# Performance work log

Measured on AMD Instinct MI355X. Metric: run time of the kernel, lower is better.

## Reference

```python
import jax, jax.numpy as jnp
import numpy as np

H = 512  # hidden_size


def setup_inputs() -> dict:
    key = jax.random.key(0)
    ks = jax.random.split(key, 12)
    B, E, S, V = 64, 512, 400, 50000
    s = 1.0 / np.sqrt(H)
    inp = {
        'embedded': jax.random.normal(ks[0], (B, E), jnp.float32),
        'hidden': jax.random.normal(ks[1], (1, B, H), jnp.float32),
        'encoder_states': jax.random.normal(ks[2], (S, B, H), jnp.float32),
        # GRU params (PyTorch layout: gates ordered r,z,n)
        'w_ih': jax.random.uniform(ks[3], (3 * H, E), jnp.float32, -s, s),
        'w_hh': jax.random.uniform(ks[4], (3 * H, H), jnp.float32, -s, s),
        'b_ih': jax.random.uniform(ks[5], (3 * H,), jnp.float32, -s, s),
        'b_hh': jax.random.uniform(ks[6], (3 * H,), jnp.float32, -s, s),
        # nn.Bilinear(H, H, 1)
        'bilin_w': jax.random.uniform(ks[7], (1, H, H), jnp.float32, -s, s),
        'bilin_b': jax.random.uniform(ks[8], (1,), jnp.float32, -s, s),
        # out: Linear(2H, V)
        'out_w': jax.random.uniform(ks[9], (V, 2 * H), jnp.float32, -1.0 / np.sqrt(2 * H), 1.0 / np.sqrt(2 * H)),
        'out_b': jax.random.uniform(ks[10], (V,), jnp.float32, -1.0 / np.sqrt(2 * H), 1.0 / np.sqrt(2 * H)),
    }
    return inp


def reference(embedded, hidden, encoder_states, w_ih, w_hh, b_ih, b_hh,
              bilin_w, bilin_b, out_w, out_b):
    h0 = hidden[0]                                   # [B, H]
    # --- single-step GRU cell (PyTorch gate order r, z, n) ---
    gi = embedded @ w_ih.T + b_ih                    # [B, 3H]
    gh = h0 @ w_hh.T + b_hh                          # [B, 3H]
    r = jax.nn.sigmoid(gi[:, :H] + gh[:, :H])
    z = jax.nn.sigmoid(gi[:, H:2 * H] + gh[:, H:2 * H])
    n = jnp.tanh(gi[:, 2 * H:] + r * gh[:, 2 * H:])
    h_new = (1.0 - z) * n + z * h0                   # [B, H]
    # --- bilinear attention: energy[s,b] = h_new[b] @ W @ enc[s,b] + bias ---
    tmp = h_new @ bilin_w[0]                         # [B, H]
    energy = jnp.einsum('bh,sbh->sb', tmp, encoder_states) + bilin_b[0]  # [S, B]
    attn = jax.nn.softmax(energy, axis=0)            # softmax over source positions
    context = jnp.einsum('sb,sbh->bh', attn, encoder_states)             # [B, H]
    combined = jnp.concatenate([h_new, context], axis=1)                 # [B, 2H]
    logits = combined @ out_w.T + out_b              # [B, V]
    logp = jax.nn.log_softmax(logits, axis=1)
    return logp, h_new[None], attn[:, :, None]
```

## Files before the change

### kernel.cpp

```cpp
#include <hip/hip_runtime.h>
#include <math.h>

static constexpr int H = 512;
static constexpr int B = 64;

typedef __bf16 bf16x8 __attribute__((ext_vector_type(8)));
typedef __bf16 bf16x4 __attribute__((ext_vector_type(4)));
typedef float f32x4 __attribute__((ext_vector_type(4)));

__global__ __launch_bounds__(256) void gemm_mfma_nt(
    const float* __restrict__ A,
    const float* __restrict__ W,
    const float* __restrict__ bias,
    float* __restrict__ C,
    int K, int N, int ldc)
{
    __shared__ __bf16 As[2][64 * 64];
    __shared__ __bf16 Ws[2][64 * 64];

    const int tid  = threadIdx.x;
    const int lane = tid & 63;
    const int wv   = tid >> 6;
    const int n0   = blockIdx.x * 64;

    const int lrow = tid >> 2;
    const int lq   = tid & 3;

    int wrow = n0 + lrow;
    if (wrow > N - 1) wrow = N - 1;
    const float* Aptr = A + (size_t)lrow * K + lq * 16;
    const float* Wptr = W + (size_t)wrow * K + lq * 16;

    f32x4 acc[4] = {};

    float4 ra[4], rw[4];
    #pragma unroll
    for (int i = 0; i < 4; ++i) {
        ra[i] = *(const float4*)(Aptr + 4 * i);
        rw[i] = *(const float4*)(Wptr + 4 * i);
    }

    const int ln = lane & 15;
    const int lk = (lane >> 4) << 3;
    const int NT = K >> 6;

    for (int t = 0; t < NT; ++t) {
        __bf16* a_s = As[t & 1];
        __bf16* w_s = Ws[t & 1];
        #pragma unroll
        for (int i = 0; i < 4; ++i) {
            const int off = ((lrow << 6) + lq * 16 + 4 * i) ^ ((lrow & 7) << 3);
            bf16x4 va = { (__bf16)ra[i].x, (__bf16)ra[i].y, (__bf16)ra[i].z, (__bf16)ra[i].w };
            bf16x4 vw = { (__bf16)rw[i].x, (__bf16)rw[i].y, (__bf16)rw[i].z, (__bf16)rw[i].w };
            *(bf16x4*)&a_s[off] = va;
            *(bf16x4*)&w_s[off] = vw;
        }
        __syncthreads();
        if (t + 1 < NT) {
            const float* Ap = Aptr + (t + 1) * 64;
            const float* Wp = Wptr + (t + 1) * 64;
            #pragma unroll
            for (int i = 0; i < 4; ++i) {
                ra[i] = *(const float4*)(Ap + 4 * i);
                rw[i] = *(const float4*)(Wp + 4 * i);
            }
        }
        bf16x8 bfrag[2];
        #pragma unroll
        for (int ks = 0; ks < 2; ++ks) {
            const int row = wv * 16 + ln;
            const int off = ((row << 6) + ks * 32 + lk) ^ ((row & 7) << 3);
            bfrag[ks] = *(bf16x8*)&w_s[off];
        }
        #pragma unroll
        for (int m = 0; m < 4; ++m) {
            const int row = m * 16 + ln;
            #pragma unroll
            for (int ks = 0; ks < 2; ++ks) {
                const int off = ((row << 6) + ks * 32 + lk) ^ ((row & 7) << 3);
                bf16x8 afrag = *(bf16x8*)&a_s[off];
                acc[m] = __builtin_amdgcn_mfma_f32_16x16x32_bf16(afrag, bfrag[ks], acc[m], 0, 0, 0);
            }
        }
    }

    const int col = n0 + wv * 16 + ln;
    if (col < N) {
        const float bv = bias ? bias[col] : 0.f;
        #pragma unroll
        for (int m = 0; m < 4; ++m) {
            const int rbase = m * 16 + (lane >> 4) * 4;
            #pragma unroll
            for (int j = 0; j < 4; ++j)
                C[(size_t)(rbase + j) * ldc + col] = acc[m][j] + bv;
        }
    }
}

__global__ __launch_bounds__(256) void gemm_a64_kn(
    const float* __restrict__ A, const float* __restrict__ W,
    float* __restrict__ C, int K, int N, int ldc)
{
    __shared__ float As[64][68];
    __shared__ float Bs[64][68];
    const int tid = threadIdx.x;
    const int n0 = blockIdx.x * 64;
    const int tv = tid & 15;
    const int tb = tid >> 4;
    const int lrow = tid >> 2;
    const int lk0  = (tid & 3) * 16;

    float acc[4][4] = {{0.f, 0.f, 0.f, 0.f}};

    for (int kc = 0; kc < K; kc += 64) {
        #pragma unroll
        for (int i = 0; i < 4; ++i) {
            const float4 a = *(const float4*)(A + (size_t)lrow * K + kc + lk0 + 4 * i);
            As[lk0 + 4 * i + 0][lrow] = a.x;
            As[lk0 + 4 * i + 1][lrow] = a.y;
            As[lk0 + 4 * i + 2][lrow] = a.z;
            As[lk0 + 4 * i + 3][lrow] = a.w;
        }
        {
            const int v  = tid & 63;
            const int kg = tid >> 6;
            #pragma unroll
            for (int i = 0; i < 16; ++i) {
                const int kk = kg * 16 + i;
                Bs[kk][v] = (n0 + v < N) ? W[(size_t)(kc + kk) * N + n0 + v] : 0.f;
            }
        }
        __syncthreads();
        #pragma unroll 16
        for (int kk = 0; kk < 64; ++kk) {
            const float4 a = *(const float4*)&As[kk][tb * 4];
            const float4 b = *(const float4*)&Bs[kk][tv * 4];
            acc[0][0] += a.x * b.x; acc[0][1] += a.x * b.y; acc[0][2] += a.x * b.z; acc[0][3] += a.x * b.w;
            acc[1][0] += a.y * b.x; acc[1][1] += a.y * b.y; acc[1][2] += a.y * b.z; acc[1][3] += a.y * b.w;
            acc[2][0] += a.z * b.x; acc[2][1] += a.z * b.y; acc[2][2] += a.z * b.z; acc[2][3] += a.z * b.w;
            acc[3][0] += a.w * b.x; acc[3][1] += a.w * b.y; acc[3][2] += a.w * b.z; acc[3][3] += a.w * b.w;
        }
        __syncthreads();
    }
    #pragma unroll
    for (int i = 0; i < 4; ++i) {
        const int bb = tb * 4 + i;
        #pragma unroll
        for (int j = 0; j < 4; ++j) {
            const int n = n0 + tv * 4 + j;
            if (n < N) C[(size_t)bb * ldc + n] = acc[i][j];
        }
    }
}

__global__ __launch_bounds__(512) void gru_gates(
    const float* __restrict__ gi, const float* __restrict__ gh,
    const float* __restrict__ h0, float* __restrict__ hnew,
    float* __restrict__ combined)
{
    const int b = blockIdx.x;
    const int h = threadIdx.x;
    const size_t o = (size_t)b * 3 * H;
    const float r = 1.f / (1.f + expf(-(gi[o + h] + gh[o + h])));
    const float z = 1.f / (1.f + expf(-(gi[o + H + h] + gh[o + H + h])));
    const float n = tanhf(gi[o + 2 * H + h] + r * gh[o + 2 * H + h]);
    const float hn = (1.f - z) * n + z * h0[(size_t)b * H + h];
    hnew[(size_t)b * H + h] = hn;
    combined[(size_t)b * 2 * H + h] = hn;
}

__global__ __launch_bounds__(256) void energy_k(
    const float* __restrict__ tmp, const float* __restrict__ enc,
    const float* __restrict__ bilin_b, float* __restrict__ energy, int S)
{
    const int gw = (int)((blockIdx.x * 256 + threadIdx.x) >> 6);
    const int lane = threadIdx.x & 63;
    if (gw >= S * B) return;
    const int s = gw >> 6;
    const int b = gw & 63;
    const float* e = enc + ((size_t)s * B + b) * H;
    const float* t = tmp + (size_t)b * H;
    const int k0 = lane * 8;
    const float4 e0 = *(const float4*)(e + k0);
    const float4 e1 = *(const float4*)(e + k0 + 4);
    const float4 t0 = *(const float4*)(t + k0);
    const float4 t1 = *(const float4*)(t + k0 + 4);
    float p = e0.x * t0.x + e0.y * t0.y + e0.z * t0.z + e0.w * t0.w
            + e1.x * t1.x + e1.y * t1.y + e1.z * t1.z + e1.w * t1.w;
    #pragma unroll
    for (int off = 32; off; off >>= 1) p += __shfl_down(p, off);
    if (lane == 0) energy[(size_t)s * B + b] = p + bilin_b[0];
}

__global__ __launch_bounds__(128) void softmax_s(
    const float* __restrict__ energy, float* __restrict__ attn, int S)
{
    const int b = blockIdx.x;
    const int t = threadIdx.x;
    __shared__ float w0[2], w1[2];
    float m = -1e30f;
    for (int s = t; s < S; s += 128) m = fmaxf(m, energy[(size_t)s * B + b]);
    #pragma unroll
    for (int off = 32; off; off >>= 1) m = fmaxf(m, __shfl_xor(m, off));
    if ((t & 63) == 0) w0[t >> 6] = m;
    __syncthreads();
    m = fmaxf(w0[0], w0[1]);
    float sum = 0.f;
    for (int s = t; s < S; s += 128) sum += expf(energy[(size_t)s * B + b] - m);
    #pragma unroll
    for (int off = 32; off; off >>= 1) sum += __shfl_xor(sum, off);
    if ((t & 63) == 0) w1[t >> 6] = sum;
    __syncthreads();
    const float inv = 1.f / (w1[0] + w1[1]);
    for (int s = t; s < S; s += 128)
        attn[(size_t)s * B + b] = expf(energy[(size_t)s * B + b] - m) * inv;
}

static constexpr int CSP = 8;
__global__ __launch_bounds__(512) void context_part(
    const float* __restrict__ attn, const float* __restrict__ enc,
    float* __restrict__ part, int S, int chunk)
{
    const int b = blockIdx.x;
    const int p = blockIdx.y;
    const int h = threadIdx.x;
    const int s0 = p * chunk;
    int s1 = s0 + chunk; if (s1 > S) s1 = S;
    __shared__ float a_s[128];
    if (h < s1 - s0) a_s[h] = attn[(size_t)(s0 + h) * B + b];
    __syncthreads();
    float c = 0.f;
    const float* e = enc + ((size_t)s0 * B + b) * H + h;
    for (int s = s0; s < s1; ++s, e += (size_t)B * H)
        c += a_s[s - s0] * (*e);
    part[((size_t)p * B + b) * H + h] = c;
}

__global__ __launch_bounds__(512) void context_reduce(
    const float* __restrict__ part, float* __restrict__ combined)
{
    const int b = blockIdx.x;
    const int h = threadIdx.x;
    float c = 0.f;
    #pragma unroll
    for (int p = 0; p < CSP; ++p) c += part[((size_t)p * B + b) * H + h];
    combined[(size_t)b * 2 * H + H + h] = c;
}

static constexpr int LSP = 16;
__global__ __launch_bounds__(256) void lsm_part(
    const float* __restrict__ logits, float* __restrict__ pm,
    float* __restrict__ ps, int V)
{
    const int b = blockIdx.x;
    const int p = blockIdx.y;
    const int t = threadIdx.x;
    const int V4 = V >> 2;
    const int chunk = (V4 + LSP - 1) / LSP;
    const int i0 = p * chunk;
    int i1 = i0 + chunk; if (i1 > V4) i1 = V4;
    const float4* row = (const float4*)(logits + (size_t)b * V);
    __shared__ float sm[4], ss[4];

    float m = -1e30f;
    for (int i = i0 + t; i < i1; i += 256) {
        const float4 v = row[i];
        m = fmaxf(fmaxf(fmaxf(m, v.x), v.y), fmaxf(v.z, v.w));
    }
    #pragma unroll
    for (int off = 32; off; off >>= 1) m = fmaxf(m, __shfl_xor(m, off));
    if ((t & 63) == 0) sm[t >> 6] = m;
    __syncthreads();
    m = fmaxf(fmaxf(sm[0], sm[1]), fmaxf(sm[2], sm[3]));

    float s = 0.f;
    for (int i = i0 + t; i < i1; i += 256) {
        const float4 v = row[i];
        s += expf(v.x - m) + expf(v.y - m) + expf(v.z - m) + expf(v.w - m);
    }
    #pragma unroll
    for (int off = 32; off; off >>= 1) s += __shfl_xor(s, off);
    if ((t & 63) == 0) ss[t >> 6] = s;
    __syncthreads();
    if (t == 0) {
        pm[b * LSP + p] = m;
        ps[b * LSP + p] = ss[0] + ss[1] + ss[2] + ss[3];
    }
}

__global__ __launch_bounds__(64) void lsm_combine(
    const float* __restrict__ pm, const float* __restrict__ ps,
    float* __restrict__ c)
{
    const int b = blockIdx.x;
    const int l = threadIdx.x;
    float m = (l < LSP) ? pm[b * LSP + l] : -1e30f;
    float mm = m;
    #pragma unroll
    for (int off = 32; off; off >>= 1) mm = fmaxf(mm, __shfl_xor(mm, off));
    float s = (l < LSP) ? ps[b * LSP + l] * expf(m - mm) : 0.f;
    #pragma unroll
    for (int off = 32; off; off >>= 1) s += __shfl_xor(s, off);
    if (l == 0) c[b] = mm + logf(s);
}

__global__ __launch_bounds__(256) void lsm_apply(
    float* __restrict__ logits, const float* __restrict__ c, int V)
{
    const int b = blockIdx.y;
    const int i = blockIdx.x * 256 + threadIdx.x;
    const int V4 = V >> 2;
    if (i >= V4) return;
    float4* row = (float4*)(logits + (size_t)b * V);
    float4 v = row[i];
    const float cb = c[b];
    v.x -= cb; v.y -= cb; v.z -= cb; v.w -= cb;
    row[i] = v;
}

extern "C" void kernel_launch(void* const* d_in, const int* in_sizes, int n_in,
                              void* d_out, int out_size, void* d_ws, size_t ws_size,
                              hipStream_t stream)
{
    const float* embedded = (const float*)d_in[0];
    const float* hidden   = (const float*)d_in[1];
    const float* enc      = (const float*)d_in[2];
    const float* w_ih     = (const float*)d_in[3];
    const float* w_hh     = (const float*)d_in[4];
    const float* b_ih     = (const float*)d_in[5];
    const float* b_hh     = (const float*)d_in[6];
    const float* bilin_w  = (const float*)d_in[7];
    const float* bilin_b  = (const float*)d_in[8];
    const float* out_w    = (const float*)d_in[9];
    const float* out_b    = (const float*)d_in[10];
    float* out = (float*)d_out;

    const int E = in_sizes[0] / B;
    const int S = in_sizes[2] / (B * H);
    const int V = in_sizes[9] / (2 * H);

    float* logp = out;
    float* hnew = out + (size_t)B * V;
    float* attn = hnew + (size_t)B * H;

    float* ws       = (float*)d_ws;
    float* gi       = ws;
    float* gh       = gi + (size_t)B * 3 * H;
    float* tmp      = gh + (size_t)B * 3 * H;
    float* energy   = tmp + (size_t)B * H;
    float* combined = energy + (size_t)S * B;
    float* part     = combined + (size_t)B * 2 * H;
    float* pm       = part + (size_t)CSP * B * H;
    float* ps       = pm + (size_t)B * LSP;
    float* cb       = ps + (size_t)B * LSP;

    gemm_mfma_nt<<<(3 * H) / 64, 256, 0, stream>>>(embedded, w_ih, b_ih, gi, E, 3 * H, 3 * H);
    gemm_mfma_nt<<<(3 * H) / 64, 256, 0, stream>>>(hidden, w_hh, b_hh, gh, H, 3 * H, 3 * H);

    gru_gates<<<B, H, 0, stream>>>(gi, gh, hidden, hnew, combined);

    gemm_a64_kn<<<H / 64, 256, 0, stream>>>(hnew, bilin_w, tmp, H, H, H);

    energy_k<<<(S * B + 3) / 4, 256, 0, stream>>>(tmp, enc, bilin_b, energy, S);

    softmax_s<<<B, 128, 0, stream>>>(energy, attn, S);

    const int chunk = (S + CSP - 1) / CSP;
    context_part<<<dim3(B, CSP), 512, 0, stream>>>(attn, enc, part, S, chunk);
    context_reduce<<<B, 512, 0, stream>>>(part, combined);

    gemm_mfma_nt<<<(V + 63) / 64, 256, 0, stream>>>(combined, out_w, out_b, logp, 2 * H, V, V);

    lsm_part<<<dim3(B, LSP), 256, 0, stream>>>(logp, pm, ps, V);
    lsm_combine<<<B, 64, 0, stream>>>(pm, ps, cb);
    lsm_apply<<<dim3((V / 4 + 255) / 256, B), 256, 0, stream>>>(logp, cb, V);
}
```

Baseline: 178.9 us.

## Fuse GRU gemms with gates, flash-style attention, wider output GEMM tile

The two GRU gate GEMMs and the gate elementwise kernel become one kernel that accumulates r, z and n tiles directly. Energy, softmax and context become a single online-softmax pass over encoder states, split into partitions, followed by a combine kernel, so the encoder tensor is read once instead of twice. The vocabulary projection GEMM now uses 128-column tiles to reuse the A tile across more outputs, and the log-softmax split count is raised. The GRU kernel loses double buffering and runs on only 8 blocks, and the flash kernel uses 64-thread blocks, which may underuse the GPU.

New measurement: 202.2 us. 1.13x slower.

```diff
diff --git a/kernel.cpp b/kernel.cpp
--- a/kernel.cpp
+++ b/kernel.cpp
@@ -3,96 +3,100 @@
 
 static constexpr int H = 512;
 static constexpr int B = 64;
+static constexpr int P = 32;
+static constexpr int LSP = 32;
 
 typedef __bf16 bf16x8 __attribute__((ext_vector_type(8)));
 typedef __bf16 bf16x4 __attribute__((ext_vector_type(4)));
 typedef float f32x4 __attribute__((ext_vector_type(4)));
 
-__global__ __launch_bounds__(256) void gemm_mfma_nt(
-    const float* __restrict__ A,
-    const float* __restrict__ W,
-    const float* __restrict__ bias,
-    float* __restrict__ C,
-    int K, int N, int ldc)
-{
-    __shared__ __bf16 As[2][64 * 64];
-    __shared__ __bf16 Ws[2][64 * 64];
-
-    const int tid  = threadIdx.x;
+__device__ __forceinline__ float sigmoidf_(float x) { return 1.f / (1.f + expf(-x)); }
+
+__global__ __launch_bounds__(256) void gru_fused(
+    const float* __restrict__ X, const float* __restrict__ Hp,
+    const float* __restrict__ w_ih, const float* __restrict__ w_hh,
+    const float* __restrict__ b_ih, const float* __restrict__ b_hh,
+    float* __restrict__ hnew, float* __restrict__ combined)
+{
+    __shared__ __bf16 As[64 * 64];
+    __shared__ __bf16 Wr[64 * 64];
+    __shared__ __bf16 Wz[64 * 64];
+    __shared__ __bf16 Wn[64 * 64];
+    const int tid = threadIdx.x;
     const int lane = tid & 63;
-    const int wv   = tid >> 6;
-    const int n0   = blockIdx.x * 64;
-
+    const int wv = tid >> 6;
+    const int c0 = blockIdx.x * 64;
     const int lrow = tid >> 2;
-    const int lq   = tid & 3;
-
-    int wrow = n0 + lrow;
-    if (wrow > N - 1) wrow = N - 1;
-    const float* Aptr = A + (size_t)lrow * K + lq * 16;
-    const float* Wptr = W + (size_t)wrow * K + lq * 16;
-
-    f32x4 acc[4] = {};
-
-    float4 ra[4], rw[4];
-    #pragma unroll
-    for (int i = 0; i < 4; ++i) {
-        ra[i] = *(const float4*)(Aptr + 4 * i);
-        rw[i] = *(const float4*)(Wptr + 4 * i);
-    }
-
+    const int lq = tid & 3;
     const int ln = lane & 15;
     const int lk = (lane >> 4) << 3;
-    const int NT = K >> 6;
-
-    for (int t = 0; t < NT; ++t) {
-        __bf16* a_s = As[t & 1];
-        __bf16* w_s = Ws[t & 1];
-        #pragma unroll
-        for (int i = 0; i < 4; ++i) {
-            const int off = ((lrow << 6) + lq * 16 + 4 * i) ^ ((lrow & 7) << 3);
-            bf16x4 va = { (__bf16)ra[i].x, (__bf16)ra[i].y, (__bf16)ra[i].z, (__bf16)ra[i].w };
-            bf16x4 vw = { (__bf16)rw[i].x, (__bf16)rw[i].y, (__bf16)rw[i].z, (__bf16)rw[i].w };
-            *(bf16x4*)&a_s[off] = va;
-            *(bf16x4*)&w_s[off] = vw;
-        }
-        __syncthreads();
-        if (t + 1 < NT) {
-            const float* Ap = Aptr + (t + 1) * 64;
-            const float* Wp = Wptr + (t + 1) * 64;
+
+    f32x4 acc_r[4] = {}, acc_z[4] = {}, acc_n[2][4] = {};
+
+    #pragma unroll
+    for (int ph = 0; ph < 2; ++ph) {
+        const float* a_src = ph ? Hp : X;
+        const float* w_src = ph ? w_hh : w_ih;
+        const float* Ap = a_src + (size_t)lrow * H + lq * 16;
+        const float* Rp = w_src + (size_t)(c0 + lrow) * H + lq * 16;
+        const float* Zp = w_src + (size_t)(H + c0 + lrow) * H + lq * 16;
+        const float* Np = w_src + (size_t)(2 * H + c0 + lrow) * H + lq * 16;
+        for (int t = 0; t < H / 64; ++t) {
+            __syncthreads();
             #pragma unroll
             for (int i = 0; i < 4; ++i) {
-                ra[i] = *(const float4*)(Ap + 4 * i);
-                rw[i] = *(const float4*)(Wp + 4 * i);
-            }
-        }
-        bf16x8 bfrag[2];
-        #pragma unroll
-        for (int ks = 0; ks < 2; ++ks) {
-            const int row = wv * 16 + ln;
-            const int off = ((row << 6) + ks * 32 + lk) ^ ((row & 7) << 3);
-            bfrag[ks] = *(bf16x8*)&w_s[off];
-        }
-        #pragma unroll
-        for (int m = 0; m < 4; ++m) {
-            const int row = m * 16 + ln;
+                const int off = ((lrow << 6) + lq * 16 + 4 * i) ^ ((lrow & 7) << 3);
+                const float4 va = *(const float4*)(Ap + t * 64 + 4 * i);
+                const float4 vr = *(const float4*)(Rp + t * 64 + 4 * i);
+                const float4 vz = *(const float4*)(Zp + t * 64 + 4 * i);
+                const float4 vn = *(const float4*)(Np + t * 64 + 4 * i);
+                *(bf16x4*)&As[off] = bf16x4{ (__bf16)va.x, (__bf16)va.y, (__bf16)va.z, (__bf16)va.w };
+                *(bf16x4*)&Wr[off] = bf16x4{ (__bf16)vr.x, (__bf16)vr.y, (__bf16)vr.z, (__bf16)vr.w };
+                *(bf16x4*)&Wz[off] = bf16x4{ (__bf16)vz.x, (__bf16)vz.y, (__bf16)vz.z, (__bf16)vz.w };
+                *(bf16x4*)&Wn[off] = bf16x4{ (__bf16)vn.x, (__bf16)vn.y, (__bf16)vn.z, (__bf16)vn.w };
+            }
+            __syncthreads();
+            bf16x8 br[2], bz[2], bn[2];
             #pragma unroll
             for (int ks = 0; ks < 2; ++ks) {
+                const int row = wv * 16 + ln;
                 const int off = ((row << 6) + ks * 32 + lk) ^ ((row & 7) << 3);
-                bf16x8 afrag = *(bf16x8*)&a_s[off];
-                acc[m] = __builtin_amdgcn_mfma_f32_16x16x32_bf16(afrag, bfrag[ks], acc[m], 0, 0, 0);
-            }
-        }
-    }
-
-    const int col = n0 + wv * 16 + ln;
-    if (col < N) {
-        const float bv = bias ? bias[col] : 0.f;
-        #pragma unroll
-        for (int m = 0; m < 4; ++m) {
-            const int rbase = m * 16 + (lane >> 4) * 4;
-            #pragma unroll
-            for (int j = 0; j < 4; ++j)
-                C[(size_t)(rbase + j) * ldc + col] = acc[m][j] + bv;
+                br[ks] = *(bf16x8*)&Wr[off];
+                bz[ks] = *(bf16x8*)&Wz[off];
+                bn[ks] = *(bf16x8*)&Wn[off];
+            }
+            #pragma unroll
+            for (int m = 0; m < 4; ++m) {
+                const int row = m * 16 + ln;
+                #pragma unroll
+                for (int ks = 0; ks < 2; ++ks) {
+                    const int off = ((row << 6) + ks * 32 + lk) ^ ((row & 7) << 3);
+                    const bf16x8 af = *(bf16x8*)&As[off];
+                    acc_r[m]     = __builtin_amdgcn_mfma_f32_16x16x32_bf16(af, br[ks], acc_r[m], 0, 0, 0);
+                    acc_z[m]     = __builtin_amdgcn_mfma_f32_16x16x32_bf16(af, bz[ks], acc_z[m], 0, 0, 0);
+                    acc_n[ph][m] = __builtin_amdgcn_mfma_f32_16x16x32_bf16(af, bn[ks], acc_n[ph][m], 0, 0, 0);
+                }
+            }
+        }
+    }
+
+    const int h = c0 + wv * 16 + ln;
+    const float br_ = b_ih[h] + b_hh[h];
+    const float bz_ = b_ih[H + h] + b_hh[H + h];
+    const float bni = b_ih[2 * H + h];
+    const float bnh = b_hh[2 * H + h];
+    #pragma unroll
+    for (int m = 0; m < 4; ++m) {
+        #pragma unroll
+        for (int j = 0; j < 4; ++j) {
+            const int b = m * 16 + (lane >> 4) * 4 + j;
+            const float r = sigmoidf_(acc_r[m][j] + br_);
+            const float z = sigmoidf_(acc_z[m][j] + bz_);
+            const float n = tanhf(acc_n[0][m][j] + bni + r * (acc_n[1][m][j] + bnh));
+            const float h0v = Hp[(size_t)b * H + h];
+            const float hn = (1.f - z) * n + z * h0v;
+            hnew[(size_t)b * H + h] = hn;
+            combined[(size_t)b * 2 * H + h] = hn;
         }
     }
 }
@@ -153,101 +157,175 @@
     }
 }
 
-__global__ __launch_bounds__(512) void gru_gates(
-    const float* __restrict__ gi, const float* __restrict__ gh,
-    const float* __restrict__ h0, float* __restrict__ hnew,
-    float* __restrict__ combined)
+__global__ __launch_bounds__(64) void flash_part(
+    const float* __restrict__ tmp, const float* __restrict__ enc,
+    const float* __restrict__ bilin_b, float* __restrict__ energy,
+    float* __restrict__ ctxp, float* __restrict__ mp, float* __restrict__ lp,
+    int S)
 {
     const int b = blockIdx.x;
-    const int h = threadIdx.x;
-    const size_t o = (size_t)b * 3 * H;
-    const float r = 1.f / (1.f + expf(-(gi[o + h] + gh[o + h])));
-    const float z = 1.f / (1.f + expf(-(gi[o + H + h] + gh[o + H + h])));
-    const float n = tanhf(gi[o + 2 * H + h] + r * gh[o + 2 * H + h]);
-    const float hn = (1.f - z) * n + z * h0[(size_t)b * H + h];
-    hnew[(size_t)b * H + h] = hn;
-    combined[(size_t)b * 2 * H + h] = hn;
-}
-
-__global__ __launch_bounds__(256) void energy_k(
-    const float* __restrict__ tmp, const float* __restrict__ enc,
-    const float* __restrict__ bilin_b, float* __restrict__ energy, int S)
-{
-    const int gw = (int)((blockIdx.x * 256 + threadIdx.x) >> 6);
-    const int lane = threadIdx.x & 63;
-    if (gw >= S * B) return;
-    const int s = gw >> 6;
-    const int b = gw & 63;
-    const float* e = enc + ((size_t)s * B + b) * H;
-    const float* t = tmp + (size_t)b * H;
-    const int k0 = lane * 8;
-    const float4 e0 = *(const float4*)(e + k0);
-    const float4 e1 = *(const float4*)(e + k0 + 4);
-    const float4 t0 = *(const float4*)(t + k0);
-    const float4 t1 = *(const float4*)(t + k0 + 4);
-    float p = e0.x * t0.x + e0.y * t0.y + e0.z * t0.z + e0.w * t0.w
-            + e1.x * t1.x + e1.y * t1.y + e1.z * t1.z + e1.w * t1.w;
-    #pragma unroll
-    for (int off = 32; off; off >>= 1) p += __shfl_down(p, off);
-    if (lane == 0) energy[(size_t)s * B + b] = p + bilin_b[0];
-}
-
-__global__ __launch_bounds__(128) void softmax_s(
-    const float* __restrict__ energy, float* __restrict__ attn, int S)
+    const int p = blockIdx.y;
+    const int ln = threadIdx.x;
+    const int k0 = ln * 8;
+
+    const float4 t0 = *(const float4*)(tmp + (size_t)b * H + k0);
+    const float4 t1 = *(const float4*)(tmp + (size_t)b * H + k0 + 4);
+    const float bb = bilin_b[0];
+
+    float m = -1e30f, l = 0.f;
+    float4 c0 = {0.f, 0.f, 0.f, 0.f}, c1 = {0.f, 0.f, 0.f, 0.f};
+
+    for (int s = p; s < S; s += P) {
+        const float* e = enc + ((size_t)s * B + b) * H + k0;
+        const float4 e0 = *(const float4*)(e);
+        const float4 e1 = *(const float4*)(e + 4);
+        float d = e0.x * t0.x + e0.y * t0.y + e0.z * t0.z + e0.w * t0.w
+                + e1.x * t1.x + e1.y * t1.y + e1.z * t1.z + e1.w * t1.w;
+        #pragma unroll
+        for (int off = 32; off; off >>= 1) d += __shfl_xor(d, off);
+        const float E = d + bb;
+        if (ln == 0) energy[(size_t)s * B + b] = E;
+        const float mn = fmaxf(m, E);
+        const float sc = expf(m - mn);
+        const float w  = expf(E - mn);
+        l = l * sc + w;
+        c0.x = c0.x * sc + w * e0.x; c0.y = c0.y * sc + w * e0.y;
+        c0.z = c0.z * sc + w * e0.z; c0.w = c0.w * sc + w * e0.w;
+        c1.x = c1.x * sc + w * e1.x; c1.y = c1.y * sc + w * e1.y;
+        c1.z = c1.z * sc + w * e1.z; c1.w = c1.w * sc + w * e1.w;
+        m = mn;
+    }
+    float* cp = ctxp + ((size_t)b * P + p) * H + k0;
+    *(float4*)cp = c0;
+    *(float4*)(cp + 4) = c1;
+    if (ln == 0) { mp[b * P + p] = m; lp[b * P + p] = l; }
+}
+
+__global__ __launch_bounds__(256) void attn_combine(
+    const float* __restrict__ mp, const float* __restrict__ lp,
+    const float* __restrict__ ctxp, const float* __restrict__ energy,
+    float* __restrict__ combined, float* __restrict__ attn, int S)
 {
     const int b = blockIdx.x;
     const int t = threadIdx.x;
-    __shared__ float w0[2], w1[2];
-    float m = -1e30f;
-    for (int s = t; s < S; s += 128) m = fmaxf(m, energy[(size_t)s * B + b]);
-    #pragma unroll
-    for (int off = 32; off; off >>= 1) m = fmaxf(m, __shfl_xor(m, off));
-    if ((t & 63) == 0) w0[t >> 6] = m;
+    __shared__ float sm_[P], sl_[P], sc_[P];
+    if (t < P) { sm_[t] = mp[b * P + t]; sl_[t] = lp[b * P + t]; }
     __syncthreads();
-    m = fmaxf(w0[0], w0[1]);
-    float sum = 0.f;
-    for (int s = t; s < S; s += 128) sum += expf(energy[(size_t)s * B + b] - m);
-    #pragma unroll
-    for (int off = 32; off; off >>= 1) sum += __shfl_xor(sum, off);
-    if ((t & 63) == 0) w1[t >> 6] = sum;
+    float M = -1e30f;
+    #pragma unroll
+    for (int p = 0; p < P; ++p) M = fmaxf(M, sm_[p]);
+    if (t < P) sc_[t] = expf(sm_[t] - M);
     __syncthreads();
-    const float inv = 1.f / (w1[0] + w1[1]);
-    for (int s = t; s < S; s += 128)
-        attn[(size_t)s * B + b] = expf(energy[(size_t)s * B + b] - m) * inv;
-}
-
-static constexpr int CSP = 8;
-__global__ __launch_bounds__(512) void context_part(
-    const float* __restrict__ attn, const float* __restrict__ enc,
-    float* __restrict__ part, int S, int chunk)
-{
-    const int b = blockIdx.x;
-    const int p = blockIdx.y;
-    const int h = threadIdx.x;
-    const int s0 = p * chunk;
-    int s1 = s0 + chunk; if (s1 > S) s1 = S;
-    __shared__ float a_s[128];
-    if (h < s1 - s0) a_s[h] = attn[(size_t)(s0 + h) * B + b];
-    __syncthreads();
-    float c = 0.f;
-    const float* e = enc + ((size_t)s0 * B + b) * H + h;
-    for (int s = s0; s < s1; ++s, e += (size_t)B * H)
-        c += a_s[s - s0] * (*e);
-    part[((size_t)p * B + b) * H + h] = c;
-}
-
-__global__ __launch_bounds__(512) void context_reduce(
-    const float* __restrict__ part, float* __restrict__ combined)
-{
-    const int b = blockIdx.x;
-    const int h = threadIdx.x;
-    float c = 0.f;
-    #pragma unroll
-    for (int p = 0; p < CSP; ++p) c += part[((size_t)p * B + b) * H + h];
-    combined[(size_t)b * 2 * H + H + h] = c;
-}
-
-static constexpr int LSP = 16;
+    float L = 0.f;
+    #pragma unroll
+    for (int p = 0; p < P; ++p) L += sl_[p] * sc_[p];
+    const float invL = 1.f / L;
+
+    for (int h = t; h < H; h += 256) {
+        float acc = 0.f;
+        #pragma unroll
+        for (int p = 0; p < P; ++p)
+            acc += ctxp[((size_t)b * P + p) * H + h] * sc_[p];
+        combined[(size_t)b * 2 * H + H + h] = acc * invL;
+    }
+    for (int s = t; s < S; s += 256)
+        attn[(size_t)s * B + b] = expf(energy[(size_t)s * B + b] - M) * invL;
+}
+
+__global__ __launch_bounds__(256) void gemm_mfma_nt128(
+    const float* __restrict__ A,
+    const float* __restrict__ W,
+    const float* __restrict__ bias,
+    float* __restrict__ C, int K, int N, int ldc)
+{
+    __shared__ __bf16 As[2][64 * 64];
+    __shared__ __bf16 Ws[2][128 * 64];
+
+    const int tid = threadIdx.x;
+    const int lane = tid & 63;
+    const int wv = tid >> 6;
+    const int n0 = blockIdx.x * 128;
+
+    const int arow = tid >> 2, aq = tid & 3;
+    const int wrow = tid >> 1, wh = tid & 1;
+    int wr = n0 + wrow;
+    if (wr > N - 1) wr = N - 1;
+    const float* Aptr = A + (size_t)arow * K + aq * 16;
+    const float* Wptr = W + (size_t)wr * K + wh * 32;
+
+    f32x4 acc[4][2] = {};
+    float4 ra[4], rw[8];
+    #pragma unroll
+    for (int i = 0; i < 4; ++i) ra[i] = *(const float4*)(Aptr + 4 * i);
+    #pragma unroll
+    for (int i = 0; i < 8; ++i) rw[i] = *(const float4*)(Wptr + 4 * i);
+
+    const int ln = lane & 15;
+    const int lk = (lane >> 4) << 3;
+    const int NT = K >> 6;
+
+    for (int t = 0; t < NT; ++t) {
+        __bf16* a_s = As[t & 1];
+        __bf16* w_s = Ws[t & 1];
+        #pragma unroll
+        for (int i = 0; i < 4; ++i) {
+            const int off = ((arow << 6) + aq * 16 + 4 * i) ^ ((arow & 7) << 3);
+            *(bf16x4*)&a_s[off] = bf16x4{ (__bf16)ra[i].x, (__bf16)ra[i].y, (__bf16)ra[i].z, (__bf16)ra[i].w };
+        }
+        #pragma unroll
+        for (int i = 0; i < 8; ++i) {
+            const int off = ((wrow << 6) + wh * 32 + 4 * i) ^ ((wrow & 7) << 3);
+            *(bf16x4*)&w_s[off] = bf16x4{ (__bf16)rw[i].x, (__bf16)rw[i].y, (__bf16)rw[i].z, (__bf16)rw[i].w };
+        }
+        __syncthreads();
+        if (t + 1 < NT) {
+            const float* Ap = Aptr + (t + 1) * 64;
+            const float* Wp = Wptr + (t + 1) * 64;
+            #pragma unroll
+            for (int i = 0; i < 4; ++i) ra[i] = *(const float4*)(Ap + 4 * i);
+            #pragma unroll
+            for (int i = 0; i < 8; ++i) rw[i] = *(const float4*)(Wp + 4 * i);
+        }
+        bf16x8 bfrag[2][2];
+        #pragma unroll
+        for (int nf = 0; nf < 2; ++nf) {
+            #pragma unroll
+            for (int ks = 0; ks < 2; ++ks) {
+                const int row = wv * 32 + nf * 16 + ln;
+                const int off = ((row << 6) + ks * 32 + lk) ^ ((row & 7) << 3);
+                bfrag[nf][ks] = *(bf16x8*)&w_s[off];
+            }
+        }
+        #pragma unroll
+        for (int m = 0; m < 4; ++m) {
+            const int row = m * 16 + ln;
+            #pragma unroll
+            for (int ks = 0; ks < 2; ++ks) {
+                const int off = ((row << 6) + ks * 32 + lk) ^ ((row & 7) << 3);
+                const bf16x8 af = *(bf16x8*)&a_s[off];
+                #pragma unroll
+                for (int nf = 0; nf < 2; ++nf)
+                    acc[m][nf] = __builtin_amdgcn_mfma_f32_16x16x32_bf16(af, bfrag[nf][ks], acc[m][nf], 0, 0, 0);
+            }
+        }
+    }
+
+    #pragma unroll
+    for (int nf = 0; nf < 2; ++nf) {
+        const int col = n0 + wv * 32 + nf * 16 + ln;
+        if (col < N) {
+            const float bv = bias[col];
+            #pragma unroll
+            for (int m = 0; m < 4; ++m) {
+                const int rbase = m * 16 + (lane >> 4) * 4;
+                #pragma unroll
+                for (int j = 0; j < 4; ++j)
+                    C[(size_t)(rbase + j) * ldc + col] = acc[m][nf][j] + bv;
+            }
+        }
+    }
+}
+
 __global__ __launch_bounds__(256) void lsm_part(
     const float* __restrict__ logits, float* __restrict__ pm,
     float* __restrict__ ps, int V)
@@ -335,7 +413,6 @@
     const float* out_b    = (const float*)d_in[10];
     float* out = (float*)d_out;
 
-    const int E = in_sizes[0] / B;
     const int S = in_sizes[2] / (B * H);
     const int V = in_sizes[9] / (2 * H);
 
@@ -344,32 +421,25 @@
     float* attn = hnew + (size_t)B * H;
 
     float* ws       = (float*)d_ws;
-    float* gi       = ws;
-    float* gh       = gi + (size_t)B * 3 * H;
-    float* tmp      = gh + (size_t)B * 3 * H;
+    float* tmp      = ws;
     float* energy   = tmp + (size_t)B * H;
     float* combined = energy + (size_t)S * B;
-    float* part     = combined + (size_t)B * 2 * H;
-    float* pm       = part + (size_t)CSP * B * H;
+    float* ctxp     = combined + (size_t)B * 2 * H;
+    float* mp       = ctxp + (size_t)B * P * H;
+    float* lp       = mp + (size_t)B * P;
+    float* pm       = lp + (size_t)B * P;
     float* ps       = pm + (size_t)B * LSP;
     float* cb       = ps + (size_t)B * LSP;
 
-    gemm_mfma_nt<<<(3 * H) / 64, 256, 0, stream>>>(embedded, w_ih, b_ih, gi, E, 3 * H, 3 * H);
-    gemm_mfma_nt<<<(3 * H) / 64, 256, 0, stream>>>(hidden, w_hh, b_hh, gh, H, 3 * H, 3 * H);
-
-    gru_gates<<<B, H, 0, stream>>>(gi, gh, hidden, hnew, combined);
+    gru_fused<<<H / 64, 256, 0, stream>>>(embedded, hidden, w_ih, w_hh, b_ih, b_hh, hnew, combined);
 
     gemm_a64_kn<<<H / 64, 256, 0, stream>>>(hnew, bilin_w, tmp, H, H, H);
 
-    energy_k<<<(S * B + 3) / 4, 256, 0, stream>>>(tmp, enc, bilin_b, energy, S);
-
-    softmax_s<<<B, 128, 0, stream>>>(energy, attn, S);
-
-    const int chunk = (S + CSP - 1) / CSP;
-    context_part<<<dim3(B, CSP), 512, 0, stream>>>(attn, enc, part, S, chunk);
-    context_reduce<<<B, 512, 0, stream>>>(part, combined);
-
-    gemm_mfma_nt<<<(V + 63) / 64, 256, 0, stream>>>(combined, out_w, out_b, logp, 2 * H, V, V);
+    flash_part<<<dim3(B, P), 64, 0, stream>>>(tmp, enc, bilin_b, energy, ctxp, mp, lp, S);
+
+    attn_combine<<<B, 256, 0, stream>>>(mp, lp, ctxp, energy, combined, attn, S);
+
+    gemm_mfma_nt128<<<(V + 127) / 128, 256, 0, stream>>>(combined, out_w, out_b, logp, 2 * H, V, V);
 
     lsm_part<<<dim3(B, LSP), 256, 0, stream>>>(logp, pm, ps, V);
     lsm_combine<<<B, 64, 0, stream>>>(pm, ps, cb);
```
